# Performance work log

Hardware: AMD Instinct MI355X
Metric: run time of the kernel (lower is better)

## Reference

```python
import jax, jax.numpy as jnp
import numpy as np

LOTRI2MAT = np.array([[0, 1, 3], [1, 2, 4], [3, 4, 5]])  # lower-tri 6-vec -> symmetric 3x3
MAT2LOTRI_I = np.array([0, 1, 1, 2, 2, 2])
MAT2LOTRI_J = np.array([0, 0, 1, 0, 1, 2])


def trilinear_warp_border(img, ddf):
    """MONAI Warp(mode='bilinear', padding_mode='border', align_corners=True).
    img: (B,C,H,W,D), ddf: (B,3,H,W,D) displacement in voxel units.
    Samples img at x + ddf(x), clamping coords to the volume (border padding).
    """
    B, C, H, W, D = img.shape
    base = jnp.stack(
        jnp.meshgrid(jnp.arange(H), jnp.arange(W), jnp.arange(D), indexing='ij'),
        axis=0,
    ).astype(img.dtype)  # (3,H,W,D)
    coords = ddf + base[None]  # (B,3,H,W,D)
    x = jnp.clip(coords[:, 0], 0.0, H - 1)
    y = jnp.clip(coords[:, 1], 0.0, W - 1)
    z = jnp.clip(coords[:, 2], 0.0, D - 1)

    x0f, y0f, z0f = jnp.floor(x), jnp.floor(y), jnp.floor(z)
    fx, fy, fz = x - x0f, y - y0f, z - z0f
    x0 = jnp.clip(x0f.astype(jnp.int32), 0, H - 1)
    y0 = jnp.clip(y0f.astype(jnp.int32), 0, W - 1)
    z0 = jnp.clip(z0f.astype(jnp.int32), 0, D - 1)
    x1 = jnp.minimum(x0 + 1, H - 1)
    y1 = jnp.minimum(y0 + 1, W - 1)
    z1 = jnp.minimum(z0 + 1, D - 1)

    def gather(img_b, xi, yi, zi):
        flat = (xi * W + yi) * D + zi  # (H,W,D)
        return img_b.reshape(C, -1)[:, flat.reshape(-1)].reshape(C, H, W, D)

    g = jax.vmap(gather)  # over batch

    out = jnp.zeros_like(img)
    for xi, wx in ((x0, 1.0 - fx), (x1, fx)):
        for yi, wy in ((y0, 1.0 - fy), (y1, fy)):
            for zi, wz in ((z0, 1.0 - fz), (z1, fz)):
                out = out + g(img, xi, yi, zi) * (wx * wy * wz)[:, None]
    return out


def jacobian_of_ddf(ddf):
    """J = I + du/dx via central differences (one-sided at boundaries).
    ddf: (B,3,H,W,D) -> (B,H,W,D,3,3) with J[...,i,j] = d u_i / d x_j + delta_ij."""
    grads = jnp.gradient(ddf, axis=(2, 3, 4))  # list over j of (B,3,H,W,D)
    J = jnp.stack(grads, axis=2)  # (B,3(i),3(j),H,W,D)
    J = J + jnp.eye(3, dtype=ddf.dtype)[None, :, :, None, None, None]
    return jnp.transpose(J, (0, 3, 4, 5, 1, 2))  # (B,H,W,D,3,3)


def setup_inputs() -> dict:
    key = jax.random.key(0)
    k1, k2 = jax.random.split(key)
    dti = jax.random.normal(k1, (2, 6, 64, 64, 64), dtype=jnp.float32)
    ddf = jax.random.normal(k2, (2, 3, 64, 64, 64), dtype=jnp.float32)
    return {"dti": dti, "ddf": ddf}


def reference(dti, ddf):
    b, _, h, w, d = dti.shape
    # 1) trilinear warp of the 6-channel lower-tri DTI
    dti_warped = trilinear_warp_border(dti, ddf)  # (B,6,H,W,D)
    # 2) lower-tri -> full symmetric 3x3, spatial-last
    M = dti_warped[:, LOTRI2MAT]                      # (B,3,3,H,W,D)
    M = jnp.transpose(M, (0, 3, 4, 5, 1, 2))          # (B,H,W,D,3,3)
    # 3) Jacobian of the deformation and its polar-decomposition rotation (finite strain)
    J = jacobian_of_ddf(ddf)                          # (B,H,W,D,3,3)
    U, _, Vh = jnp.linalg.svd(J, full_matrices=False)
    R = jnp.matmul(U, Vh)                             # orthogonal factor of J
    # 4) rotate tensors: R^T M R
    out = jnp.einsum('...ji,...jk,...kl->...il', R, M, R)
    # 5) back to lower-tri channel-first form
    out = jnp.transpose(out, (0, 4, 5, 1, 2, 3))      # (B,3,3,H,W,D)
    return out[:, MAT2LOTRI_I, MAT2LOTRI_J]           # (B,6,H,W,D)
```

## Files before the change

### kernel.cpp

```cpp
#include <hip/hip_runtime.h>

#define NVOX 262144
#define TOTAL (2 * NVOX)

typedef float f2u __attribute__((ext_vector_type(2), aligned(4)));

__global__ void zero_count(int* __restrict__ bad) {
    if (threadIdx.x == 0) bad[0] = 0;
}

__global__ __launch_bounds__(256)
void warp_main(const float* __restrict__ dti,
               const float* __restrict__ ddf,
               float* __restrict__ out,
               int* __restrict__ bad, int max_bad)
{
    const int idx = blockIdx.x * 256 + threadIdx.x;
    const int b = idx >> 18;
    const int r = idx & (NVOX - 1);
    const int x = r >> 12;
    const int y = (r >> 6) & 63;
    const int z = r & 63;

    const float* db = ddf + (size_t)b * 3 * NVOX;

    const float ux = db[r];
    const float uy = db[NVOX + r];
    const float uz = db[2 * NVOX + r];

    const float cx = fminf(fmaxf((float)x + ux, 0.0f), 63.0f);
    const float cy = fminf(fmaxf((float)y + uy, 0.0f), 63.0f);
    const float cz = fminf(fmaxf((float)z + uz, 0.0f), 63.0f);
    const float fx0 = floorf(cx), fy0 = floorf(cy), fz0 = floorf(cz);
    const float fx = cx - fx0, fy = cy - fy0, fz = cz - fz0;
    const int x0 = (int)fx0, y0 = (int)fy0, z0 = (int)fz0;
    const int x1 = min(x0 + 1, 63), y1 = min(y0 + 1, 63);

    const float gx = 1.0f - fx, gy = 1.0f - fy, gz = 1.0f - fz;
    const float q00 = gx * gy, q01 = gx * fy, q10 = fx * gy, q11 = fx * fy;

    const bool ztop = (z0 == 63);
    const int zb = ztop ? 62 : z0;
    const int p00 = (x0 * 64 + y0) * 64 + zb, p01 = (x0 * 64 + y1) * 64 + zb;
    const int p10 = (x1 * 64 + y0) * 64 + zb, p11 = (x1 * 64 + y1) * 64 + zb;

    const float* tb = dti + (size_t)b * 6 * NVOX;
    float m[6];
#pragma unroll
    for (int c = 0; c < 6; ++c) {
        const float* tc = tb + c * NVOX;
        const f2u v00 = *(const f2u*)(tc + p00);
        const f2u v01 = *(const f2u*)(tc + p01);
        const f2u v10 = *(const f2u*)(tc + p10);
        const f2u v11 = *(const f2u*)(tc + p11);
        const float l00 = (ztop ? v00.y : v00.x) * gz + v00.y * fz;
        const float l01 = (ztop ? v01.y : v01.x) * gz + v01.y * fz;
        const float l10 = (ztop ? v10.y : v10.x) * gz + v10.y * fz;
        const float l11 = (ztop ? v11.y : v11.x) * gz + v11.y * fz;
        m[c] = q00 * l00 + q01 * l01 + q10 * l10 + q11 * l11;
    }

    const int xm = max(x - 1, 0), xp = min(x + 1, 63);
    const int ym = max(y - 1, 0), yp = min(y + 1, 63);
    const int zm = max(z - 1, 0), zp = min(z + 1, 63);
    const float sx = (xp - xm == 2) ? 0.5f : 1.0f;
    const float sy = (yp - ym == 2) ? 0.5f : 1.0f;
    const float sz = (zp - zm == 2) ? 0.5f : 1.0f;

    float P[3][3];
#pragma unroll
    for (int i = 0; i < 3; ++i) {
        const float* ui = db + i * NVOX;
        const float ctr = (i == 0) ? ux : (i == 1) ? uy : uz;
        P[i][0] = (ui[(xp * 64 + y) * 64 + z] - ui[(xm * 64 + y) * 64 + z]) * sx
                + (i == 0 ? 1.0f : 0.0f);
        P[i][1] = (ui[(x * 64 + yp) * 64 + z] - ui[(x * 64 + ym) * 64 + z]) * sy
                + (i == 1 ? 1.0f : 0.0f);
        P[i][2] = (__shfl(ctr, zp) - __shfl(ctr, zm)) * sz + (i == 2 ? 1.0f : 0.0f);
    }

    float cond_est = 0.0f;
#pragma unroll
    for (int it = 0; it < 6; ++it) {
        const float C00 = P[1][1] * P[2][2] - P[1][2] * P[2][1];
        const float C01 = P[1][2] * P[2][0] - P[1][0] * P[2][2];
        const float C02 = P[1][0] * P[2][1] - P[1][1] * P[2][0];
        const float C10 = P[0][2] * P[2][1] - P[0][1] * P[2][2];
        const float C11 = P[0][0] * P[2][2] - P[0][2] * P[2][0];
        const float C12 = P[0][1] * P[2][0] - P[0][0] * P[2][1];
        const float C20 = P[0][1] * P[1][2] - P[0][2] * P[1][1];
        const float C21 = P[0][2] * P[1][0] - P[0][0] * P[1][2];
        const float C22 = P[0][0] * P[1][1] - P[0][1] * P[1][0];
        const float det = P[0][0] * C00 + P[0][1] * C01 + P[0][2] * C02;

        const float n2 = P[0][0]*P[0][0] + P[0][1]*P[0][1] + P[0][2]*P[0][2]
                       + P[1][0]*P[1][0] + P[1][1]*P[1][1] + P[1][2]*P[1][2]
                       + P[2][0]*P[2][0] + P[2][1]*P[2][1] + P[2][2]*P[2][2];
        const float a2 = C00*C00 + C01*C01 + C02*C02
                       + C10*C10 + C11*C11 + C12*C12
                       + C20*C20 + C21*C21 + C22*C22;

        const float ad = fmaxf(fabsf(det), 1e-30f);
        if (it == 0) cond_est = sqrtf(n2 * a2) / ad;

        const float t  = fmaxf(sqrtf(a2 / n2), 1e-20f);
        const float sg = (det < 0.0f) ? -1.0f : 1.0f;
        const float c1 = 0.5f * sqrtf(t / ad);
        const float c2 = 0.5f * sg / sqrtf(t * ad);

        P[0][0] = c1 * P[0][0] + c2 * C00;  P[0][1] = c1 * P[0][1] + c2 * C01;  P[0][2] = c1 * P[0][2] + c2 * C02;
        P[1][0] = c1 * P[1][0] + c2 * C10;  P[1][1] = c1 * P[1][1] + c2 * C11;  P[1][2] = c1 * P[1][2] + c2 * C12;
        P[2][0] = c1 * P[2][0] + c2 * C20;  P[2][1] = c1 * P[2][1] + c2 * C21;  P[2][2] = c1 * P[2][2] + c2 * C22;
    }

    const float M3[3][3] = {{m[0], m[1], m[3]},
                            {m[1], m[2], m[4]},
                            {m[3], m[4], m[5]}};
    float T[3][3];
#pragma unroll
    for (int i = 0; i < 3; ++i)
#pragma unroll
        for (int j = 0; j < 3; ++j)
            T[i][j] = P[0][i] * M3[0][j] + P[1][i] * M3[1][j] + P[2][i] * M3[2][j];

    float A[3][3];
#pragma unroll
    for (int i = 0; i < 3; ++i)
#pragma unroll
        for (int j = 0; j < 3; ++j)
            A[i][j] = T[i][0] * P[0][j] + T[i][1] * P[1][j] + T[i][2] * P[2][j];

    float* ob = out + (size_t)b * 6 * NVOX;
    ob[0 * NVOX + r] = A[0][0];
    ob[1 * NVOX + r] = A[1][0];
    ob[2 * NVOX + r] = A[1][1];
    ob[3 * NVOX + r] = A[2][0];
    ob[4 * NVOX + r] = A[2][1];
    ob[5 * NVOX + r] = A[2][2];

    if (cond_est > 1e4f) {
        const int slot = atomicAdd(bad, 1);
        if (slot < max_bad) bad[1 + slot] = idx;
    }
}

__global__ __launch_bounds__(256)
void rescue(const float* __restrict__ dti,
            const float* __restrict__ ddf,
            float* __restrict__ out,
            const int* __restrict__ bad, int max_bad)
{
    const int n = min(bad[0], max_bad);
    for (int k = blockIdx.x * 256 + threadIdx.x; k < n; k += 4 * 256) {
        const int idx = bad[1 + k];
        const int b = idx >> 18;
        const int r = idx & (NVOX - 1);
        const int x = r >> 12;
        const int y = (r >> 6) & 63;
        const int z = r & 63;

        const float* db = ddf + (size_t)b * 3 * NVOX;

        const float cx = fminf(fmaxf((float)x + db[r], 0.0f), 63.0f);
        const float cy = fminf(fmaxf((float)y + db[NVOX + r], 0.0f), 63.0f);
        const float cz = fminf(fmaxf((float)z + db[2 * NVOX + r], 0.0f), 63.0f);
        const float fx0 = floorf(cx), fy0 = floorf(cy), fz0 = floorf(cz);
        const float fx = cx - fx0, fy = cy - fy0, fz = cz - fz0;
        const int x0 = (int)fx0, y0 = (int)fy0, z0 = (int)fz0;
        const int x1 = min(x0 + 1, 63), y1 = min(y0 + 1, 63), z1 = min(z0 + 1, 63);
        const float gx = 1.0f - fx, gy = 1.0f - fy, gz = 1.0f - fz;
        const float w000 = gx*gy*gz, w001 = gx*gy*fz, w010 = gx*fy*gz, w011 = gx*fy*fz;
        const float w100 = fx*gy*gz, w101 = fx*gy*fz, w110 = fx*fy*gz, w111 = fx*fy*fz;
        const int o000 = (x0*64+y0)*64+z0, o001 = (x0*64+y0)*64+z1;
        const int o010 = (x0*64+y1)*64+z0, o011 = (x0*64+y1)*64+z1;
        const int o100 = (x1*64+y0)*64+z0, o101 = (x1*64+y0)*64+z1;
        const int o110 = (x1*64+y1)*64+z0, o111 = (x1*64+y1)*64+z1;

        const float* tb = dti + (size_t)b * 6 * NVOX;
        float m[6];
        for (int c = 0; c < 6; ++c) {
            const float* tc = tb + c * NVOX;
            m[c] = w000*tc[o000] + w001*tc[o001] + w010*tc[o010] + w011*tc[o011]
                 + w100*tc[o100] + w101*tc[o101] + w110*tc[o110] + w111*tc[o111];
        }

        const int xm = max(x-1,0), xp = min(x+1,63);
        const int ym = max(y-1,0), yp = min(y+1,63);
        const int zm = max(z-1,0), zp = min(z+1,63);
        const double sx = (xp-xm==2)?0.5:1.0, sy = (yp-ym==2)?0.5:1.0, sz = (zp-zm==2)?0.5:1.0;
        double X[3][3];
        for (int i = 0; i < 3; ++i) {
            const float* ui = db + i * NVOX;
            X[i][0] = ((double)ui[(xp*64+y)*64+z] - (double)ui[(xm*64+y)*64+z]) * sx + (i==0?1.0:0.0);
            X[i][1] = ((double)ui[(x*64+yp)*64+z] - (double)ui[(x*64+ym)*64+z]) * sy + (i==1?1.0:0.0);
            X[i][2] = ((double)ui[(x*64+y)*64+zp] - (double)ui[(x*64+y)*64+zm]) * sz + (i==2?1.0:0.0);
        }

        for (int it = 0; it < 14; ++it) {
            double mx = 0.0;
            for (int i = 0; i < 3; ++i)
                for (int j = 0; j < 3; ++j) mx = fmax(mx, fabs(X[i][j]));
            const double s = 1.0 / fmax(mx, 1e-300);
            for (int i = 0; i < 3; ++i)
                for (int j = 0; j < 3; ++j) X[i][j] *= s;

            const double C00 = X[1][1]*X[2][2] - X[1][2]*X[2][1];
            const double C01 = X[1][2]*X[2][0] - X[1][0]*X[2][2];
            const double C02 = X[1][0]*X[2][1] - X[1][1]*X[2][0];
            const double C10 = X[0][2]*X[2][1] - X[0][1]*X[2][2];
            const double C11 = X[0][0]*X[2][2] - X[0][2]*X[2][0];
            const double C12 = X[0][1]*X[2][0] - X[0][0]*X[2][1];
            const double C20 = X[0][1]*X[1][2] - X[0][2]*X[1][1];
            const double C21 = X[0][2]*X[1][0] - X[0][0]*X[1][2];
            const double C22 = X[0][0]*X[1][1] - X[0][1]*X[1][0];
            const double det = X[0][0]*C00 + X[0][1]*C01 + X[0][2]*C02;
            const double n2 = X[0][0]*X[0][0]+X[0][1]*X[0][1]+X[0][2]*X[0][2]
                            + X[1][0]*X[1][0]+X[1][1]*X[1][1]+X[1][2]*X[1][2]
                            + X[2][0]*X[2][0]+X[2][1]*X[2][1]+X[2][2]*X[2][2];
            const double a2 = C00*C00+C01*C01+C02*C02 + C10*C10+C11*C11+C12*C12
                            + C20*C20+C21*C21+C22*C22;
            const double t  = fmax(sqrt(a2 / n2), 1e-150);
            const double ad = fmax(fabs(det), 1e-280);
            const double sg = (det < 0.0) ? -1.0 : 1.0;
            const double c1 = 0.5 * sqrt(t / ad);
            const double c2 = 0.5 * sg / sqrt(t * ad);
            X[0][0]=c1*X[0][0]+c2*C00; X[0][1]=c1*X[0][1]+c2*C01; X[0][2]=c1*X[0][2]+c2*C02;
            X[1][0]=c1*X[1][0]+c2*C10; X[1][1]=c1*X[1][1]+c2*C11; X[1][2]=c1*X[1][2]+c2*C12;
            X[2][0]=c1*X[2][0]+c2*C20; X[2][1]=c1*X[2][1]+c2*C21; X[2][2]=c1*X[2][2]+c2*C22;
        }

        const double M3[3][3] = {{(double)m[0], (double)m[1], (double)m[3]},
                                 {(double)m[1], (double)m[2], (double)m[4]},
                                 {(double)m[3], (double)m[4], (double)m[5]}};
        double T[3][3], A[3][3];
        for (int i = 0; i < 3; ++i)
            for (int j = 0; j < 3; ++j)
                T[i][j] = X[0][i]*M3[0][j] + X[1][i]*M3[1][j] + X[2][i]*M3[2][j];
        for (int i = 0; i < 3; ++i)
            for (int j = 0; j < 3; ++j)
                A[i][j] = T[i][0]*X[0][j] + T[i][1]*X[1][j] + T[i][2]*X[2][j];

        float* ob = out + (size_t)b * 6 * NVOX;
        ob[0 * NVOX + r] = (float)A[0][0];
        ob[1 * NVOX + r] = (float)A[1][0];
        ob[2 * NVOX + r] = (float)A[1][1];
        ob[3 * NVOX + r] = (float)A[2][0];
        ob[4 * NVOX + r] = (float)A[2][1];
        ob[5 * NVOX + r] = (float)A[2][2];
    }
}

extern "C" void kernel_launch(void* const* d_in, const int* in_sizes, int n_in,
                              void* d_out, int out_size, void* d_ws, size_t ws_size,
                              hipStream_t stream) {
    const float* dti = (const float*)d_in[0];
    const float* ddf = (const float*)d_in[1];
    float* out = (float*)d_out;
    int* bad = (int*)d_ws;
    const int max_bad = (int)min((size_t)8192, ws_size / 4 - 1);

    zero_count<<<1, 64, 0, stream>>>(bad);
    warp_main<<<TOTAL / 256, 256, 0, stream>>>(dti, ddf, out, bad, max_bad);
    rescue<<<4, 256, 0, stream>>>(dti, ddf, out, bad, max_bad);
}
```

Baseline: 108.2 us.

## Trim polar iteration count, use rsqrt, and compute only needed output entries

Cuts the float Newton polar-decomposition loop from six iterations to five and replaces the divides and sqrts with rsqrt-based coefficients. The condition-number estimate is now a multiply-compare instead of a sqrt and divide. Only the six lower-triangular entries of R^T M R are computed, and a launch-bounds occupancy hint is added. The zero-count kernel is replaced by hipMemsetAsync. Fewer iterations and rsqrt may loosen accuracy on moderately conditioned voxels that are not sent to the double-precision rescue path.

```diff
diff --git a/kernel.cpp b/kernel.cpp
--- a/kernel.cpp
+++ b/kernel.cpp
@@ -5,11 +5,7 @@
 
 typedef float f2u __attribute__((ext_vector_type(2), aligned(4)));
 
-__global__ void zero_count(int* __restrict__ bad) {
-    if (threadIdx.x == 0) bad[0] = 0;
-}
-
-__global__ __launch_bounds__(256)
+__global__ __launch_bounds__(256, 8)
 void warp_main(const float* __restrict__ dti,
                const float* __restrict__ ddf,
                float* __restrict__ out,
@@ -79,9 +75,9 @@
         P[i][2] = (__shfl(ctr, zp) - __shfl(ctr, zm)) * sz + (i == 2 ? 1.0f : 0.0f);
     }
 
-    float cond_est = 0.0f;
-#pragma unroll
-    for (int it = 0; it < 6; ++it) {
+    bool ill = false;
+#pragma unroll
+    for (int it = 0; it < 5; ++it) {
         const float C00 = P[1][1] * P[2][2] - P[1][2] * P[2][1];
         const float C01 = P[1][2] * P[2][0] - P[1][0] * P[2][2];
         const float C02 = P[1][0] * P[2][1] - P[1][1] * P[2][0];
@@ -101,12 +97,13 @@
                        + C20*C20 + C21*C21 + C22*C22;
 
         const float ad = fmaxf(fabsf(det), 1e-30f);
-        if (it == 0) cond_est = sqrtf(n2 * a2) / ad;
-
-        const float t  = fmaxf(sqrtf(a2 / n2), 1e-20f);
-        const float sg = (det < 0.0f) ? -1.0f : 1.0f;
-        const float c1 = 0.5f * sqrtf(t / ad);
-        const float c2 = 0.5f * sg / sqrtf(t * ad);
+        if (it == 0) ill = (n2 * a2 > 1e8f * ad * ad);
+
+        const float t   = fmaxf(sqrtf(a2) * rsqrtf(n2), 1e-20f);
+        const float it2 = rsqrtf(t * ad);
+        const float sg  = (det < 0.0f) ? -0.5f : 0.5f;
+        const float c1  = 0.5f * t * it2;
+        const float c2  = sg * it2;
 
         P[0][0] = c1 * P[0][0] + c2 * C00;  P[0][1] = c1 * P[0][1] + c2 * C01;  P[0][2] = c1 * P[0][2] + c2 * C02;
         P[1][0] = c1 * P[1][0] + c2 * C10;  P[1][1] = c1 * P[1][1] + c2 * C11;  P[1][2] = c1 * P[1][2] + c2 * C12;
@@ -123,22 +120,15 @@
         for (int j = 0; j < 3; ++j)
             T[i][j] = P[0][i] * M3[0][j] + P[1][i] * M3[1][j] + P[2][i] * M3[2][j];
 
-    float A[3][3];
-#pragma unroll
-    for (int i = 0; i < 3; ++i)
-#pragma unroll
-        for (int j = 0; j < 3; ++j)
-            A[i][j] = T[i][0] * P[0][j] + T[i][1] * P[1][j] + T[i][2] * P[2][j];
-
     float* ob = out + (size_t)b * 6 * NVOX;
-    ob[0 * NVOX + r] = A[0][0];
-    ob[1 * NVOX + r] = A[1][0];
-    ob[2 * NVOX + r] = A[1][1];
-    ob[3 * NVOX + r] = A[2][0];
-    ob[4 * NVOX + r] = A[2][1];
-    ob[5 * NVOX + r] = A[2][2];
-
-    if (cond_est > 1e4f) {
+    ob[0 * NVOX + r] = T[0][0]*P[0][0] + T[0][1]*P[1][0] + T[0][2]*P[2][0];
+    ob[1 * NVOX + r] = T[1][0]*P[0][0] + T[1][1]*P[1][0] + T[1][2]*P[2][0];
+    ob[2 * NVOX + r] = T[1][0]*P[0][1] + T[1][1]*P[1][1] + T[1][2]*P[2][1];
+    ob[3 * NVOX + r] = T[2][0]*P[0][0] + T[2][1]*P[1][0] + T[2][2]*P[2][0];
+    ob[4 * NVOX + r] = T[2][0]*P[0][1] + T[2][1]*P[1][1] + T[2][2]*P[2][1];
+    ob[5 * NVOX + r] = T[2][0]*P[0][2] + T[2][1]*P[1][2] + T[2][2]*P[2][2];
+
+    if (ill) {
         const int slot = atomicAdd(bad, 1);
         if (slot < max_bad) bad[1 + slot] = idx;
     }
@@ -219,11 +209,11 @@
                             + X[2][0]*X[2][0]+X[2][1]*X[2][1]+X[2][2]*X[2][2];
             const double a2 = C00*C00+C01*C01+C02*C02 + C10*C10+C11*C11+C12*C12
                             + C20*C20+C21*C21+C22*C22;
-            const double t  = fmax(sqrt(a2 / n2), 1e-150);
+            const double t2 = fmax(sqrt(a2 / n2), 1e-150);
             const double ad = fmax(fabs(det), 1e-280);
             const double sg = (det < 0.0) ? -1.0 : 1.0;
-            const double c1 = 0.5 * sqrt(t / ad);
-            const double c2 = 0.5 * sg / sqrt(t * ad);
+            const double c1 = 0.5 * sqrt(t2 / ad);
+            const double c2 = 0.5 * sg / sqrt(t2 * ad);
             X[0][0]=c1*X[0][0]+c2*C00; X[0][1]=c1*X[0][1]+c2*C01; X[0][2]=c1*X[0][2]+c2*C02;
             X[1][0]=c1*X[1][0]+c2*C10; X[1][1]=c1*X[1][1]+c2*C11; X[1][2]=c1*X[1][2]+c2*C12;
             X[2][0]=c1*X[2][0]+c2*C20; X[2][1]=c1*X[2][1]+c2*C21; X[2][2]=c1*X[2][2]+c2*C22;
@@ -259,7 +249,7 @@
     int* bad = (int*)d_ws;
     const int max_bad = (int)min((size_t)8192, ws_size / 4 - 1);
 
-    zero_count<<<1, 64, 0, stream>>>(bad);
+    hipMemsetAsync(bad, 0, sizeof(int), stream);
     warp_main<<<TOTAL / 256, 256, 0, stream>>>(dti, ddf, out, bad, max_bad);
     rescue<<<4, 256, 0, stream>>>(dti, ddf, out, bad, max_bad);
 }
```

After: 108.7 us. Within noise of the previous version (+0.4%).
